# Optimization experiments

Hardware: AMD Instinct MI355X
Metric: run time of the kernel (lower is better)

The kernel has to match this reference:

```python
import jax, jax.numpy as jnp
import numpy as np

N_WIRES = 24
DIM = 2
N_LAYERS = 4  # brickwork layers -> 12+11+12+11 = 46 two-qubit gates


def _brick_pairs():
    pairs = []
    for layer in range(N_LAYERS):
        start = layer % 2
        for w in range(start, N_WIRES - 1, 2):
            pairs.append((w, w + 1))
    return np.asarray(pairs, dtype=np.int64)  # (46, 2)


def setup_inputs() -> dict:
    key = jax.random.key(0)
    k1, k2 = jax.random.split(key)
    gate_wires = _brick_pairs()
    n_gates = gate_wires.shape[0]
    # per-wire initial state vectors (AbstractState -> one free index per wire)
    states = jax.random.normal(k1, (N_WIRES, DIM), dtype=jnp.float32)
    # two-qubit gates, axis order (in0, out0, in1, out1) per subscripts_unitary
    gates = jax.random.normal(k2, (n_gates, DIM, DIM, DIM, DIM), dtype=jnp.float32)
    return {"states": states, "gates": gates, "gate_wires": gate_wires}


def reference(states, gates, gate_wires):
    # Equivalent to jnp.einsum(subscripts_unitary(circuit), *tensors):
    # outer-product of initial per-wire states, then sequential contraction
    # of each gate's input axes (0, 2) with the state's wire axes.
    n_wires = states.shape[0]
    wires = np.asarray(gate_wires)
    psi = states[0]
    for w in range(1, n_wires):  # fixed structural loop over wires
        psi = jnp.tensordot(psi, states[w], axes=0)  # -> (d,)*n_wires
    for g in range(gates.shape[0]):  # fixed structural loop over gates
        w0, w1 = int(wires[g, 0]), int(wires[g, 1])
        # gate axes: 0=in0, 1=out0, 2=in1, 3=out1
        psi = jnp.tensordot(gates[g], psi, axes=[[0, 2], [w0, w1]])
        # result axes: (out0, out1, remaining wires); restore wire ordering
        psi = jnp.moveaxis(psi, (0, 1), (w0, w1))
    return psi  # final statevector, shape (d,)*n_wires
```

## Files before the change

### kernel.cpp

```cpp
#include <hip/hip_runtime.h>


#define SWZ(j) ((j) ^ (((j) >> 6) & 15) ^ ((((j) >> 10) & 1) << 4))
#define DEL(x, S) (((x) & ((1 << (S)) - 1)) | (((x) >> ((S) + 1)) << (S)))

template<int B0, int B1>
__device__ __forceinline__ void gate_sc(float v[64], const float* __restrict__ g) {
  float m[16];
#pragma unroll
  for (int vv = 0; vv < 4; ++vv)
#pragma unroll
    for (int uu = 0; uu < 4; ++uu)
      m[vv * 4 + uu] = g[(uu >> 1) * 8 + (vv >> 1) * 4 + (uu & 1) * 2 + (vv & 1)];
  constexpr int S1 = 1 << B0;
  constexpr int S0 = 1 << B1;
#pragma unroll
  for (int b = 0; b < 64; ++b) {
    if (b & (S0 | S1)) continue;
    const float a0 = v[b], a1 = v[b + S1], a2 = v[b + S0], a3 = v[b + S0 + S1];
    v[b]           = m[0]  * a0 + m[1]  * a1 + m[2]  * a2 + m[3]  * a3;
    v[b + S1]      = m[4]  * a0 + m[5]  * a1 + m[6]  * a2 + m[7]  * a3;
    v[b + S0]      = m[8]  * a0 + m[9]  * a1 + m[10] * a2 + m[11] * a3;
    v[b + S0 + S1] = m[12] * a0 + m[13] * a1 + m[14] * a2 + m[15] * a3;
  }
}

#define JB1(t, r) ((t) | ((r) << 8))
#define JM1(t, r) (((t) & 15) | ((((r) >> 1) & 15) << 4) | (((r) & 1) << 8) | (((r) >> 5) << 9) | (((t) >> 4) << 10))
#define JA1(t, r) (((r) & 3) | ((((r) >> 3) & 7) << 2) | ((((r) >> 2) & 1) << 5) | ((t) << 6))
#define JW1(t, r) (((t) & 31) | ((((r) >> 2) & 1) << 5) | (((r) & 1) << 6) | ((((r) >> 1) & 1) << 7) | ((((r) >> 3) & 7) << 8) | (((t) >> 5) << 11))
#define JF(t, r)  (((r) & 3) | ((t) << 2) | (((r) >> 2) << 10))
#define JV(t, r)  (((t) & 127) | (((r) & 1) << 7) | ((((r) >> 1) & 1) << 8) | ((((r) >> 3) & 1) << 9) | ((((r) >> 2) & 1) << 10) | ((((r) >> 4) & 3) << 11) | (((t) >> 7) << 13))
#define JW2(t, r) (((t) & 31) | ((((r) >> 1) & 7) << 5) | (((r) & 1) << 8) | ((((r) >> 4) & 3) << 9) | (((t) >> 5) << 11))

#define TRANS(JW, JR, S, RBIT)                                        \
  do {                                                                \
    _Pragma("unroll")                                                 \
    for (int r = 0; r < 64; ++r) if ((((r) >> (RBIT)) & 1) == 0)      \
      buf[DEL(SWZ(JW(t, r)), S)] = v[r];                              \
    __syncthreads();                                                  \
    _Pragma("unroll")                                                 \
    for (int r = 0; r < 64; ++r) if ((((r) >> (RBIT)) & 1) == 0)      \
      v[r] = buf[DEL(SWZ(JR(t, r)), S)];                              \
    __syncthreads();                                                  \
    _Pragma("unroll")                                                 \
    for (int r = 0; r < 64; ++r) if ((((r) >> (RBIT)) & 1) == 1)      \
      buf[DEL(SWZ(JW(t, r)), S)] = v[r];                              \
    __syncthreads();                                                  \
    _Pragma("unroll")                                                 \
    for (int r = 0; r < 64; ++r) if ((((r) >> (RBIT)) & 1) == 1)      \
      v[r] = buf[DEL(SWZ(JR(t, r)), S)];                              \
    __syncthreads();                                                  \
  } while (0)

__global__ __launch_bounds__(256) void k_pass1(
    const float* __restrict__ states, const float* __restrict__ gates,
    float* __restrict__ out) {
  __shared__ float buf[8192];
  const int t = threadIdx.x;
  const int b = blockIdx.x;

  {
    float p = 1.f;
    for (int k = 0; k < 8; ++k) p *= states[(23 - k) * 2 + ((t >> k) & 1)];
    buf[t] = p;
    if (t < 64) {
      float q = 1.f;
      for (int k = 0; k < 6; ++k) q *= states[(15 - k) * 2 + ((t >> k) & 1)];
      buf[256 + t] = q;
    }
  }
  float pref = 1.f;
  for (int k = 0; k < 10; ++k) pref *= states[(9 - k) * 2 + ((b >> k) & 1)];
  __syncthreads();

  float v[64];
  const float plT = pref * buf[t];
#pragma unroll
  for (int r = 0; r < 64; ++r) v[r] = plT * buf[256 + r];
  __syncthreads();

  gate_sc<4, 5>(v, gates + 16 * 5);
  gate_sc<2, 3>(v, gates + 16 * 6);
  gate_sc<0, 1>(v, gates + 16 * 7);
  gate_sc<3, 4>(v, gates + 16 * 17);
  gate_sc<1, 2>(v, gates + 16 * 18);
  gate_sc<2, 3>(v, gates + 16 * 29);
  TRANS(JB1, JM1, 8, 0);
  gate_sc<3, 4>(v, gates + 16 * 8);
  gate_sc<1, 2>(v, gates + 16 * 9);
  gate_sc<4, 0>(v, gates + 16 * 19);
  gate_sc<2, 3>(v, gates + 16 * 20);
  gate_sc<0, 5>(v, gates + 16 * 30);
  gate_sc<3, 4>(v, gates + 16 * 31);
  TRANS(JM1, JA1, 5, 2);
  gate_sc<3, 4>(v, gates + 16 * 10);
  gate_sc<0, 1>(v, gates + 16 * 11);
  gate_sc<4, 5>(v, gates + 16 * 21);
  gate_sc<1, 3>(v, gates + 16 * 22);
  gate_sc<5, 2>(v, gates + 16 * 32);
  gate_sc<3, 4>(v, gates + 16 * 33);
  gate_sc<0, 1>(v, gates + 16 * 34);
  gate_sc<4, 5>(v, gates + 16 * 44);
  gate_sc<1, 3>(v, gates + 16 * 45);
  TRANS(JA1, JW1, 5, 2);
  gate_sc<4, 5>(v, gates + 16 * 41);
  gate_sc<1, 3>(v, gates + 16 * 42);
  gate_sc<2, 0>(v, gates + 16 * 43);

  const long long ob = ((long long)b) << 14;
#pragma unroll
  for (int r = 0; r < 64; ++r) out[ob | JW1(t, r)] = v[r];
}

__global__ __launch_bounds__(256) void k_pass2a(
    const float* __restrict__ gates, float* __restrict__ out) {
  __shared__ float buf[8192];
  const int t = threadIdx.x;
  const int b = blockIdx.x;
  const long long base0 = (((long long)(b >> 4)) << 18) | ((long long)(b & 15) << 6);

  float v[64];
#pragma unroll
  for (int c = 0; c < 16; ++c) {
    float4 x = *(const float4*)(&out[base0 + ((t & 15) << 2) + ((t >> 4) << 10) + ((long long)c << 14)]);
    v[4 * c] = x.x; v[4 * c + 1] = x.y; v[4 * c + 2] = x.z; v[4 * c + 3] = x.w;
  }
  gate_sc<4, 5>(v, gates + 16 * 3);
  TRANS(JF, JV, 10, 2);
  gate_sc<2, 4>(v, gates + 16 * 4);
  gate_sc<4, 5>(v, gates + 16 * 15);
  gate_sc<3, 2>(v, gates + 16 * 16);
  gate_sc<2, 4>(v, gates + 16 * 27);
  gate_sc<1, 3>(v, gates + 16 * 28);
  gate_sc<3, 2>(v, gates + 16 * 39);
  gate_sc<0, 1>(v, gates + 16 * 40);

#pragma unroll
  for (int r = 0; r < 64; ++r) {
    const int j = JV(t, r);
    out[base0 | (((long long)(j >> 6)) << 10) | (j & 63)] = v[r];
  }
}

__global__ __launch_bounds__(256) void k_pass2b(
    const float* __restrict__ gates, float* __restrict__ out) {
  __shared__ float buf[8192];
  const int t = threadIdx.x;
  const int b = blockIdx.x;

  float v[64];
#pragma unroll
  for (int c = 0; c < 16; ++c) {
    float4 x = *(const float4*)(&out[((t & 7) << 2) + ((long long)b << 5) + ((t >> 3) << 15) + ((long long)c << 20)]);
    v[4 * c] = x.x; v[4 * c + 1] = x.y; v[4 * c + 2] = x.z; v[4 * c + 3] = x.w;
  }
  gate_sc<4, 5>(v, gates + 16 * 0);
  gate_sc<2, 3>(v, gates + 16 * 1);
  gate_sc<3, 4>(v, gates + 16 * 12);
  gate_sc<4, 5>(v, gates + 16 * 23);
  TRANS(JF, JB1, 10, 2);
  gate_sc<0, 1>(v, gates + 16 * 2);
  gate_sc<1, 2>(v, gates + 16 * 13);
  gate_sc<2, 3>(v, gates + 16 * 24);
  gate_sc<3, 4>(v, gates + 16 * 35);
  TRANS(JB1, JW2, 8, 0);
  gate_sc<3, 0>(v, gates + 16 * 14);
  gate_sc<0, 4>(v, gates + 16 * 25);
  gate_sc<2, 3>(v, gates + 16 * 26);
  gate_sc<4, 5>(v, gates + 16 * 36);
  gate_sc<3, 0>(v, gates + 16 * 37);
  gate_sc<1, 2>(v, gates + 16 * 38);

#pragma unroll
  for (int r = 0; r < 64; ++r) {
    const int j = JW2(t, r);
    out[(((long long)(j >> 5)) << 15) | ((long long)b << 5) | (j & 31)] = v[r];
  }
}

extern "C" void kernel_launch(void* const* d_in, const int* in_sizes, int n_in,
                              void* d_out, int out_size, void* d_ws, size_t ws_size,
                              hipStream_t stream) {
  const float* states = (const float*)d_in[0];
  const float* gates = (const float*)d_in[1];
  float* out = (float*)d_out;

  k_pass1<<<1024, 256, 0, stream>>>(states, gates, out);
  k_pass2a<<<1024, 256, 0, stream>>>(gates, out);
  k_pass2b<<<1024, 256, 0, stream>>>(gates, out);
}
```

Measured before the change: 188.9 us.

## Split pass2 kernels into 128-thread blocks over 13-qubit tiles with new swizzle

The two second-phase kernels now work on 8192-amplitude tiles with 128 threads and a 4096-float shared buffer instead of 16384-amplitude tiles with 256 threads, launching twice as many blocks. The qubit-to-thread/register mappings, the global load/store addressing and the shared-memory swizzle are redone for the smaller tile, and in pass2a two gates are moved ahead of the transpose. The aim is more resident blocks per CU and less LDS per block, which should help latency hiding. In exchange, global access segments become narrower (16 floats instead of 32 in pass2b), which may hurt coalescing.

```diff
diff --git a/kernel.cpp b/kernel.cpp
--- a/kernel.cpp
+++ b/kernel.cpp
@@ -2,6 +2,7 @@
 
 
 #define SWZ(j) ((j) ^ (((j) >> 6) & 15) ^ ((((j) >> 10) & 1) << 4))
+#define SWZ13(j) ((j) ^ (((j) >> 5) & 31) ^ ((((j) >> 9) & 1) << 1) ^ ((((j) >> 10) & 1) << 4))
 #define DEL(x, S) (((x) & ((1 << (S)) - 1)) | (((x) >> ((S) + 1)) << (S)))
 
 template<int B0, int B1>
@@ -29,9 +30,11 @@
 #define JM1(t, r) (((t) & 15) | ((((r) >> 1) & 15) << 4) | (((r) & 1) << 8) | (((r) >> 5) << 9) | (((t) >> 4) << 10))
 #define JA1(t, r) (((r) & 3) | ((((r) >> 3) & 7) << 2) | ((((r) >> 2) & 1) << 5) | ((t) << 6))
 #define JW1(t, r) (((t) & 31) | ((((r) >> 2) & 1) << 5) | (((r) & 1) << 6) | ((((r) >> 1) & 1) << 7) | ((((r) >> 3) & 7) << 8) | (((t) >> 5) << 11))
-#define JF(t, r)  (((r) & 3) | ((t) << 2) | (((r) >> 2) << 10))
-#define JV(t, r)  (((t) & 127) | (((r) & 1) << 7) | ((((r) >> 1) & 1) << 8) | ((((r) >> 3) & 1) << 9) | ((((r) >> 2) & 1) << 10) | ((((r) >> 4) & 3) << 11) | (((t) >> 7) << 13))
-#define JW2(t, r) (((t) & 31) | ((((r) >> 1) & 7) << 5) | (((r) & 1) << 8) | ((((r) >> 4) & 3) << 9) | (((t) >> 5) << 11))
+
+#define JF2(t, r) (((r) & 3) | (((t) & 127) << 2) | (((r) >> 2) << 9))
+#define JPA(t, r) (((t) & 63) | (((r) & 1) << 6) | ((((r) >> 1) & 1) << 7) | ((((r) >> 3) & 1) << 8) | ((((r) >> 2) & 1) << 9) | ((((r) >> 4) & 3) << 10) | (((t) >> 6) << 12))
+#define JP1(t, r) (((t) & 127) | ((r) << 7))
+#define JP2(t, r) (((t) & 15) | ((((r) >> 1) & 7) << 4) | (((r) & 1) << 7) | ((((r) >> 4) & 3) << 8) | (((t) >> 4) << 10))
 
 #define TRANS(JW, JR, S, RBIT)                                        \
   do {                                                                \
@@ -50,6 +53,26 @@
     _Pragma("unroll")                                                 \
     for (int r = 0; r < 64; ++r) if ((((r) >> (RBIT)) & 1) == 1)      \
       v[r] = buf[DEL(SWZ(JR(t, r)), S)];                              \
+    __syncthreads();                                                  \
+  } while (0)
+
+#define TRANS13(JW, JR, S, RBIT)                                      \
+  do {                                                                \
+    _Pragma("unroll")                                                 \
+    for (int r = 0; r < 64; ++r) if ((((r) >> (RBIT)) & 1) == 0)      \
+      buf[DEL(SWZ13(JW(t, r)), S)] = v[r];                            \
+    __syncthreads();                                                  \
+    _Pragma("unroll")                                                 \
+    for (int r = 0; r < 64; ++r) if ((((r) >> (RBIT)) & 1) == 0)      \
+      v[r] = buf[DEL(SWZ13(JR(t, r)), S)];                            \
+    __syncthreads();                                                  \
+    _Pragma("unroll")                                                 \
+    for (int r = 0; r < 64; ++r) if ((((r) >> (RBIT)) & 1) == 1)      \
+      buf[DEL(SWZ13(JW(t, r)), S)] = v[r];                            \
+    __syncthreads();                                                  \
+    _Pragma("unroll")                                                 \
+    for (int r = 0; r < 64; ++r) if ((((r) >> (RBIT)) & 1) == 1)      \
+      v[r] = buf[DEL(SWZ13(JR(t, r)), S)];                            \
     __syncthreads();                                                  \
   } while (0)
 
@@ -113,23 +136,23 @@
   for (int r = 0; r < 64; ++r) out[ob | JW1(t, r)] = v[r];
 }
 
-__global__ __launch_bounds__(256) void k_pass2a(
+__global__ __launch_bounds__(128) void k_pass2a(
     const float* __restrict__ gates, float* __restrict__ out) {
-  __shared__ float buf[8192];
+  __shared__ float buf[4096];
   const int t = threadIdx.x;
   const int b = blockIdx.x;
-  const long long base0 = (((long long)(b >> 4)) << 18) | ((long long)(b & 15) << 6);
+  const long long base0 = ((long long)(b & 31) << 6) | ((long long)(b >> 5) << 18);
 
   float v[64];
 #pragma unroll
   for (int c = 0; c < 16; ++c) {
-    float4 x = *(const float4*)(&out[base0 + ((t & 15) << 2) + ((t >> 4) << 10) + ((long long)c << 14)]);
+    float4 x = *(const float4*)(&out[base0 + ((t & 15) << 2) + ((long long)((t >> 4) | (c << 3)) << 11)]);
     v[4 * c] = x.x; v[4 * c + 1] = x.y; v[4 * c + 2] = x.z; v[4 * c + 3] = x.w;
   }
   gate_sc<4, 5>(v, gates + 16 * 3);
-  TRANS(JF, JV, 10, 2);
-  gate_sc<2, 4>(v, gates + 16 * 4);
-  gate_sc<4, 5>(v, gates + 16 * 15);
+  gate_sc<2, 3>(v, gates + 16 * 4);
+  gate_sc<3, 4>(v, gates + 16 * 15);
+  TRANS13(JF2, JPA, 9, 2);
   gate_sc<3, 2>(v, gates + 16 * 16);
   gate_sc<2, 4>(v, gates + 16 * 27);
   gate_sc<1, 3>(v, gates + 16 * 28);
@@ -138,33 +161,33 @@
 
 #pragma unroll
   for (int r = 0; r < 64; ++r) {
-    const int j = JV(t, r);
-    out[base0 | (((long long)(j >> 6)) << 10) | (j & 63)] = v[r];
-  }
-}
-
-__global__ __launch_bounds__(256) void k_pass2b(
+    const int j = JPA(t, r);
+    out[base0 | (j & 63) | ((long long)(j >> 6) << 11)] = v[r];
+  }
+}
+
+__global__ __launch_bounds__(128) void k_pass2b(
     const float* __restrict__ gates, float* __restrict__ out) {
-  __shared__ float buf[8192];
+  __shared__ float buf[4096];
   const int t = threadIdx.x;
   const int b = blockIdx.x;
 
   float v[64];
 #pragma unroll
   for (int c = 0; c < 16; ++c) {
-    float4 x = *(const float4*)(&out[((t & 7) << 2) + ((long long)b << 5) + ((t >> 3) << 15) + ((long long)c << 20)]);
+    float4 x = *(const float4*)(&out[((t & 3) << 2) + ((long long)b << 4) + ((long long)((t >> 2) | (c << 5)) << 15)]);
     v[4 * c] = x.x; v[4 * c + 1] = x.y; v[4 * c + 2] = x.z; v[4 * c + 3] = x.w;
   }
   gate_sc<4, 5>(v, gates + 16 * 0);
   gate_sc<2, 3>(v, gates + 16 * 1);
   gate_sc<3, 4>(v, gates + 16 * 12);
   gate_sc<4, 5>(v, gates + 16 * 23);
-  TRANS(JF, JB1, 10, 2);
+  TRANS13(JF2, JP1, 10, 3);
   gate_sc<0, 1>(v, gates + 16 * 2);
   gate_sc<1, 2>(v, gates + 16 * 13);
   gate_sc<2, 3>(v, gates + 16 * 24);
   gate_sc<3, 4>(v, gates + 16 * 35);
-  TRANS(JB1, JW2, 8, 0);
+  TRANS13(JP1, JP2, 7, 0);
   gate_sc<3, 0>(v, gates + 16 * 14);
   gate_sc<0, 4>(v, gates + 16 * 25);
   gate_sc<2, 3>(v, gates + 16 * 26);
@@ -174,8 +197,8 @@
 
 #pragma unroll
   for (int r = 0; r < 64; ++r) {
-    const int j = JW2(t, r);
-    out[(((long long)(j >> 5)) << 15) | ((long long)b << 5) | (j & 31)] = v[r];
+    const int j = JP2(t, r);
+    out[(j & 15) | ((long long)b << 4) | ((long long)(j >> 4) << 15)] = v[r];
   }
 }
 
@@ -187,6 +210,6 @@
   float* out = (float*)d_out;
 
   k_pass1<<<1024, 256, 0, stream>>>(states, gates, out);
-  k_pass2a<<<1024, 256, 0, stream>>>(gates, out);
-  k_pass2b<<<1024, 256, 0, stream>>>(gates, out);
-}
+  k_pass2a<<<2048, 128, 0, stream>>>(gates, out);
+  k_pass2b<<<2048, 128, 0, stream>>>(gates, out);
+}
```

Result: slower. 198.1 us (+4.8%).

## Rework pass2 transposes into four-stage shared-memory exchanges with new index mappings

Applied to the files above, without the earlier changes.

The two second-pass kernels get new in-register bit layouts and new load and store address mappings, and gates are regrouped around the exchanges. Each shared-memory transpose is split into four quarter stages so the LDS buffer halves, and it uses a new XOR swizzle, which could raise occupancy. Pass2a now loads 128-element contiguous runs and writes with float2 stores. The cost is more barriers per transpose, and the hand-derived bit mappings are a correctness risk.

```diff
diff --git a/kernel.cpp b/kernel.cpp
--- a/kernel.cpp
+++ b/kernel.cpp
@@ -29,9 +29,6 @@
 #define JM1(t, r) (((t) & 15) | ((((r) >> 1) & 15) << 4) | (((r) & 1) << 8) | (((r) >> 5) << 9) | (((t) >> 4) << 10))
 #define JA1(t, r) (((r) & 3) | ((((r) >> 3) & 7) << 2) | ((((r) >> 2) & 1) << 5) | ((t) << 6))
 #define JW1(t, r) (((t) & 31) | ((((r) >> 2) & 1) << 5) | (((r) & 1) << 6) | ((((r) >> 1) & 1) << 7) | ((((r) >> 3) & 7) << 8) | (((t) >> 5) << 11))
-#define JF(t, r)  (((r) & 3) | ((t) << 2) | (((r) >> 2) << 10))
-#define JV(t, r)  (((t) & 127) | (((r) & 1) << 7) | ((((r) >> 1) & 1) << 8) | ((((r) >> 3) & 1) << 9) | ((((r) >> 2) & 1) << 10) | ((((r) >> 4) & 3) << 11) | (((t) >> 7) << 13))
-#define JW2(t, r) (((t) & 31) | ((((r) >> 1) & 7) << 5) | (((r) & 1) << 8) | ((((r) >> 4) & 3) << 9) | (((t) >> 5) << 11))
 
 #define TRANS(JW, JR, S, RBIT)                                        \
   do {                                                                \
@@ -52,6 +49,28 @@
       v[r] = buf[DEL(SWZ(JR(t, r)), S)];                              \
     __syncthreads();                                                  \
   } while (0)
+
+#define T4STAGE(JW, JR, RA, RB, SA, SB, BIDX)                         \
+    _Pragma("unroll")                                                 \
+    for (int r = 0; r < 64; ++r)                                      \
+      if (((((r) >> (RA)) & 1) == (SA)) && ((((r) >> (RB)) & 1) == (SB))) \
+        buf[BIDX(JW(t, r))] = v[r];                                   \
+    __syncthreads();                                                  \
+    _Pragma("unroll")                                                 \
+    for (int r = 0; r < 64; ++r)                                      \
+      if (((((r) >> (RA)) & 1) == (SA)) && ((((r) >> (RB)) & 1) == (SB))) \
+        v[r] = buf[BIDX(JR(t, r))];                                   \
+    __syncthreads();
+
+#define TRANS4(JW, JR, RA, RB, BIDX)                                  \
+  do {                                                                \
+    T4STAGE(JW, JR, RA, RB, 0, 0, BIDX)                               \
+    T4STAGE(JW, JR, RA, RB, 0, 1, BIDX)                               \
+    T4STAGE(JW, JR, RA, RB, 1, 0, BIDX)                               \
+    T4STAGE(JW, JR, RA, RB, 1, 1, BIDX)                               \
+  } while (0)
+
+#define BSWZ(x) ((x) ^ (((x) >> 5) & 31))
 
 __global__ __launch_bounds__(256) void k_pass1(
     const float* __restrict__ states, const float* __restrict__ gates,
@@ -113,69 +132,82 @@
   for (int r = 0; r < 64; ++r) out[ob | JW1(t, r)] = v[r];
 }
 
+#define JF3(t, r) (((r) & 3) | (((t) & 255) << 2) | (((r) >> 2) << 10))
+#define JW2A(t, r) (((r) & 1) | (((t) & 63) << 1) | ((((r) >> 1) & 1) << 7) | ((((r) >> 3) & 1) << 8) | ((((r) >> 4) & 1) << 9) | ((((r) >> 2) & 1) << 10) | ((((r) >> 5) & 1) << 11) | ((((t) >> 6) & 1) << 12) | ((((t) >> 7) & 1) << 13))
+#define BIDX_A(j) BSWZ(DEL(DEL((j), 10), 0))
+
 __global__ __launch_bounds__(256) void k_pass2a(
     const float* __restrict__ gates, float* __restrict__ out) {
-  __shared__ float buf[8192];
+  __shared__ float buf[4096];
   const int t = threadIdx.x;
   const int b = blockIdx.x;
-  const long long base0 = (((long long)(b >> 4)) << 18) | ((long long)(b & 15) << 6);
+  const long long base0 = ((long long)(b & 15) << 7) | ((long long)(b >> 4) << 18);
 
   float v[64];
 #pragma unroll
   for (int c = 0; c < 16; ++c) {
-    float4 x = *(const float4*)(&out[base0 + ((t & 15) << 2) + ((t >> 4) << 10) + ((long long)c << 14)]);
+    const int jb = (c << 10) | (t << 2);
+    float4 x = *(const float4*)(&out[base0 + (jb & 127) + ((long long)(jb >> 7) << 11)]);
     v[4 * c] = x.x; v[4 * c + 1] = x.y; v[4 * c + 2] = x.z; v[4 * c + 3] = x.w;
   }
   gate_sc<4, 5>(v, gates + 16 * 3);
-  TRANS(JF, JV, 10, 2);
-  gate_sc<2, 4>(v, gates + 16 * 4);
-  gate_sc<4, 5>(v, gates + 16 * 15);
-  gate_sc<3, 2>(v, gates + 16 * 16);
-  gate_sc<2, 4>(v, gates + 16 * 27);
-  gate_sc<1, 3>(v, gates + 16 * 28);
-  gate_sc<3, 2>(v, gates + 16 * 39);
-  gate_sc<0, 1>(v, gates + 16 * 40);
-
-#pragma unroll
-  for (int r = 0; r < 64; ++r) {
-    const int j = JV(t, r);
-    out[base0 | (((long long)(j >> 6)) << 10) | (j & 63)] = v[r];
-  }
-}
+  gate_sc<2, 3>(v, gates + 16 * 4);
+  gate_sc<3, 4>(v, gates + 16 * 15);
+  TRANS4(JF3, JW2A, 2, 0, BIDX_A);
+  gate_sc<4, 2>(v, gates + 16 * 16);
+  gate_sc<2, 5>(v, gates + 16 * 27);
+  gate_sc<3, 4>(v, gates + 16 * 28);
+  gate_sc<4, 2>(v, gates + 16 * 39);
+  gate_sc<1, 3>(v, gates + 16 * 40);
+
+#pragma unroll
+  for (int h = 0; h < 32; ++h) {
+    const int j = JW2A(t, 2 * h);
+    float2 w2; w2.x = v[2 * h]; w2.y = v[2 * h + 1];
+    *(float2*)(&out[base0 + (j & 127) + ((long long)(j >> 7) << 11)]) = w2;
+  }
+}
+
+#define JW1B(t, r) (((r) & 1) | (((t) & 127) << 1) | ((((r) >> 1) & 1) << 8) | ((((r) >> 2) & 1) << 9) | ((((r) >> 3) & 1) << 10) | ((((r) >> 5) & 1) << 11) | ((((r) >> 4) & 1) << 12) | ((((t) >> 7) & 1) << 13))
+#define JW2B(t, r) (((t) & 31) | (((r) & 1) << 5) | ((((r) >> 4) & 1) << 6) | ((((r) >> 3) & 1) << 7) | ((((r) >> 1) & 1) << 8) | ((((r) >> 2) & 1) << 9) | ((((r) >> 5) & 1) << 10) | ((((t) >> 5) & 1) << 11) | ((((t) >> 6) & 1) << 12) | ((((t) >> 7) & 1) << 13))
+#define BIDX_B1(j) BSWZ(DEL(DEL((j), 12), 0))
+#define BIDX_B2(j) BSWZ(DEL(DEL((j), 9), 8))
 
 __global__ __launch_bounds__(256) void k_pass2b(
     const float* __restrict__ gates, float* __restrict__ out) {
-  __shared__ float buf[8192];
+  __shared__ float buf[4096];
   const int t = threadIdx.x;
   const int b = blockIdx.x;
+  const long long bb = (long long)b << 5;
 
   float v[64];
 #pragma unroll
   for (int c = 0; c < 16; ++c) {
-    float4 x = *(const float4*)(&out[((t & 7) << 2) + ((long long)b << 5) + ((t >> 3) << 15) + ((long long)c << 20)]);
+    const int jb = (c << 10) | (t << 2);
+    float4 x = *(const float4*)(&out[(jb & 31) + bb + ((long long)(jb >> 5) << 15)]);
     v[4 * c] = x.x; v[4 * c + 1] = x.y; v[4 * c + 2] = x.z; v[4 * c + 3] = x.w;
   }
   gate_sc<4, 5>(v, gates + 16 * 0);
   gate_sc<2, 3>(v, gates + 16 * 1);
   gate_sc<3, 4>(v, gates + 16 * 12);
   gate_sc<4, 5>(v, gates + 16 * 23);
-  TRANS(JF, JB1, 10, 2);
-  gate_sc<0, 1>(v, gates + 16 * 2);
-  gate_sc<1, 2>(v, gates + 16 * 13);
-  gate_sc<2, 3>(v, gates + 16 * 24);
-  gate_sc<3, 4>(v, gates + 16 * 35);
-  TRANS(JB1, JW2, 8, 0);
-  gate_sc<3, 0>(v, gates + 16 * 14);
-  gate_sc<0, 4>(v, gates + 16 * 25);
-  gate_sc<2, 3>(v, gates + 16 * 26);
-  gate_sc<4, 5>(v, gates + 16 * 36);
-  gate_sc<3, 0>(v, gates + 16 * 37);
-  gate_sc<1, 2>(v, gates + 16 * 38);
+  TRANS4(JF3, JW1B, 4, 0, BIDX_B1);
+  gate_sc<1, 2>(v, gates + 16 * 2);
+  gate_sc<2, 3>(v, gates + 16 * 13);
+  gate_sc<3, 5>(v, gates + 16 * 24);
+  gate_sc<5, 4>(v, gates + 16 * 35);
+  TRANS4(JW1B, JW2B, 2, 1, BIDX_B2);
+  gate_sc<3, 1>(v, gates + 16 * 14);
+  gate_sc<1, 2>(v, gates + 16 * 25);
+  gate_sc<4, 3>(v, gates + 16 * 26);
+  gate_sc<2, 5>(v, gates + 16 * 36);
+  gate_sc<3, 1>(v, gates + 16 * 37);
+  gate_sc<0, 4>(v, gates + 16 * 38);
 
 #pragma unroll
   for (int r = 0; r < 64; ++r) {
-    const int j = JW2(t, r);
-    out[(((long long)(j >> 5)) << 15) | ((long long)b << 5) | (j & 31)] = v[r];
+    const int j = JW2B(t, r);
+    out[(j & 31) + bb + ((long long)(j >> 5) << 15)] = v[r];
   }
 }
 
```

Measured after the change: 183.8 us. 2.7% less time.
